# Kernel tuning notes

Hardware: AMD Instinct MI355X
Metric: run time of the kernel (lower is better)

The kernel has to match this reference:

```python
import jax, jax.numpy as jnp
import numpy as np

IN_FEATURES = 4096
OUT_FEATURES = 14336
TOKENS = 32


def setup_inputs() -> dict:
    key = jax.random.key(0)
    k1, k2, k3 = jax.random.split(key, 3)
    x = jax.random.normal(k1, (TOKENS, IN_FEATURES), dtype=jnp.float32)
    # int8-valued quantized weight stored as int32 (symmetric Q8, range [-127, 127])
    weight = jax.random.randint(k2, (OUT_FEATURES, IN_FEATURES), -127, 128, dtype=jnp.int32)
    # per-in-feature (per-column of [out,in] matrix) positive scales
    scales = jax.random.uniform(k3, (IN_FEATURES,), dtype=jnp.float32, minval=0.001, maxval=0.02)
    return {"x": x, "weight": weight, "scales": scales}


def reference(x, weight, scales):
    # Original torch: dequant[o,i] = weight[o,i] * scales[i]; out = x @ dequant.T
    # Equivalent fused form: out[t,o] = sum_i (x[t,i]*scales[i]) * weight[o,i]
    x_scaled = x * scales[None, :]            # [T, in]
    w = weight.astype(jnp.float32)            # [out, in]
    out = jnp.einsum('ti,oi->to', x_scaled, w)  # [T, out]
    return out
```

## Files before the change

kernel.cpp:

```cpp
#include <hip/hip_runtime.h>
#include <stdint.h>
#include <stddef.h>

#define IN_F   4096
#define OUT_F  14336
#define TOK    32

#define OTILE  16
#define KWAVE  (IN_F / 4)
#define KBW    (KWAVE / 32)

typedef __attribute__((ext_vector_type(8))) short bf16x8;
typedef __attribute__((ext_vector_type(4))) float f32x4;

__global__ __launch_bounds__(256) void prep_kernel(
    const float* __restrict__ x, const float* __restrict__ scales,
    int4* __restrict__ xfrag)
{
    const int f = blockIdx.x * 256 + threadIdx.x;
    const int t  = f >> 9;
    const int i8 = f & 511;
    const int kb = i8 >> 2;
    const int kg = i8 & 3;
    const float4* xp = (const float4*)(x + (size_t)t * IN_F + i8 * 8);
    const float4* sp = (const float4*)(scales + i8 * 8);
    float4 x0 = xp[0], x1 = xp[1];
    float4 s0 = sp[0], s1 = sp[1];
    float v[8] = { x0.x*s0.x, x0.y*s0.y, x0.z*s0.z, x0.w*s0.w,
                   x1.x*s1.x, x1.y*s1.y, x1.z*s1.z, x1.w*s1.w };
    uint32_t h[8];
#pragma unroll
    for (int j = 0; j < 8; ++j) {
        uint32_t b = __float_as_uint(v[j]);
        b += 0x7fffu + ((b >> 16) & 1u);
        h[j] = b >> 16;
    }
    int4 d;
    d.x = (int)(h[0] | (h[1] << 16));
    d.y = (int)(h[2] | (h[3] << 16));
    d.z = (int)(h[4] | (h[5] << 16));
    d.w = (int)(h[6] | (h[7] << 16));
    xfrag[((kb * 2 + (t >> 4)) * 64) + kg * 16 + (t & 15)] = d;
}

__global__ __launch_bounds__(256, 4) void qgemm_kernel(
    const int* __restrict__ wgt, const int4* __restrict__ xfrag,
    float* __restrict__ out)
{
    __shared__ float lred[4][8][64];
    const int lane = threadIdx.x & 63;
    const int wv   = threadIdx.x >> 6;
    const int lx   = lane & 15;
    const int quad = lane >> 4;
    const int o0   = blockIdx.x * OTILE;

    const int* wp = wgt + (size_t)(o0 + lx) * IN_F + wv * KWAVE + quad * 8;
    const int4* ap = xfrag + ((size_t)wv * KBW) * 2 * 64 + lane;

    f32x4 acc[2] = { {0.f,0.f,0.f,0.f}, {0.f,0.f,0.f,0.f} };

#pragma unroll 8
    for (int kb = 0; kb < KBW; ++kb) {
        int4 av0 = ap[(kb * 2 + 0) * 64];
        int4 av1 = ap[(kb * 2 + 1) * 64];
        const int4 w0 = *(const int4*)(wp + kb * 32);
        const int4 w1 = *(const int4*)(wp + kb * 32 + 4);
        bf16x8 b;
        b[0] = (short)(__float_as_uint((float)w0.x) >> 16);
        b[1] = (short)(__float_as_uint((float)w0.y) >> 16);
        b[2] = (short)(__float_as_uint((float)w0.z) >> 16);
        b[3] = (short)(__float_as_uint((float)w0.w) >> 16);
        b[4] = (short)(__float_as_uint((float)w1.x) >> 16);
        b[5] = (short)(__float_as_uint((float)w1.y) >> 16);
        b[6] = (short)(__float_as_uint((float)w1.z) >> 16);
        b[7] = (short)(__float_as_uint((float)w1.w) >> 16);
        bf16x8 a0, a1;
        __builtin_memcpy(&a0, &av0, 16);
        __builtin_memcpy(&a1, &av1, 16);
        acc[0] = __builtin_amdgcn_mfma_f32_16x16x32_bf16(a0, b, acc[0], 0, 0, 0);
        acc[1] = __builtin_amdgcn_mfma_f32_16x16x32_bf16(a1, b, acc[1], 0, 0, 0);
    }

#pragma unroll
    for (int s = 0; s < 8; ++s)
        lred[wv][s][lane] = acc[s >> 2][s & 3];
    __syncthreads();

    if (wv == 0) {
#pragma unroll
        for (int s = 0; s < 8; ++s) {
            const float v = lred[0][s][lane] + lred[1][s][lane]
                          + lred[2][s][lane] + lred[3][s][lane];
            const int t = (s >> 2) * 16 + quad * 4 + (s & 3);
            out[(size_t)t * OUT_F + o0 + lx] = v;
        }
    }
}

extern "C" void kernel_launch(void* const* d_in, const int* in_sizes, int n_in,
                              void* d_out, int out_size, void* d_ws, size_t ws_size,
                              hipStream_t stream)
{
    const float* x      = (const float*)d_in[0];
    const int*   wgt    = (const int*)d_in[1];
    const float* scales = (const float*)d_in[2];
    float* out = (float*)d_out;
    int4*  xfrag = (int4*)d_ws;

    prep_kernel<<<dim3((TOK * IN_F / 8) / 256), 256, 0, stream>>>(x, scales, xfrag);

    qgemm_kernel<<<dim3(OUT_F / OTILE), 256, 0, stream>>>(wgt, xfrag, out);
}
```

Before: 336.0 us.

## Stage weight tiles through double-buffered LDS via global_load_lds

Weight rows are now copied asynchronously from global memory into a double-buffered LDS tile with global_load_lds, 512 columns per chunk. Each chunk is consumed from LDS while the next one is prefetched, which replaces the per-lane strided global int4 loads. The goal is to make the weight stream (the dominant bytes, int32 weights) coalesced and overlapped with compute. In exchange the kernel adds a barrier per chunk, uses a large LDS footprint that lowers occupancy to 2 blocks per CU, and keeps the int32 weight traffic unchanged.

```diff
diff --git a/kernel.cpp b/kernel.cpp
--- a/kernel.cpp
+++ b/kernel.cpp
@@ -7,9 +7,14 @@
 #define TOK    32
 
 #define OTILE  16
-#define KWAVE  (IN_F / 4)
-#define KBW    (KWAVE / 32)
+#define CHUNK  512
+#define NCH    (IN_F / CHUNK)
+#define KBC    (CHUNK / 32)
+#define KBW    (KBC / 4)
+#define ROWPAD 516
 
+typedef const __attribute__((address_space(1))) void* gas_ptr;
+typedef __attribute__((address_space(3))) void* las_ptr;
 typedef __attribute__((ext_vector_type(8))) short bf16x8;
 typedef __attribute__((ext_vector_type(4))) float f32x4;
 
@@ -43,42 +48,67 @@
     xfrag[((kb * 2 + (t >> 4)) * 64) + kg * 16 + (t & 15)] = d;
 }
 
-__global__ __launch_bounds__(256, 4) void qgemm_kernel(
+__global__ __launch_bounds__(256, 2) void qgemm_kernel(
     const int* __restrict__ wgt, const int4* __restrict__ xfrag,
     float* __restrict__ out)
 {
+    __shared__ int   wbuf[2][OTILE * ROWPAD];
     __shared__ float lred[4][8][64];
     const int lane = threadIdx.x & 63;
     const int wv   = threadIdx.x >> 6;
+    const int wvu  = __builtin_amdgcn_readfirstlane(wv);
     const int lx   = lane & 15;
     const int quad = lane >> 4;
     const int o0   = blockIdx.x * OTILE;
 
-    const int* wp = wgt + (size_t)(o0 + lx) * IN_F + wv * KWAVE + quad * 8;
-    const int4* ap = xfrag + ((size_t)wv * KBW) * 2 * 64 + lane;
+    auto stage = [&](int buf, int c) {
+#pragma unroll
+        for (int rr = 0; rr < 4; ++rr) {
+            const int r = wvu * 4 + rr;
+            const int* src = wgt + (size_t)(o0 + r) * IN_F + c * CHUNK
+                                 + lane * 4;
+            int* dst = &wbuf[buf][r * ROWPAD];
+            __builtin_amdgcn_global_load_lds((gas_ptr)src, (las_ptr)dst, 16, 0, 0);
+            __builtin_amdgcn_global_load_lds((gas_ptr)(src + 256),
+                                             (las_ptr)(dst + 256), 16, 0, 0);
+        }
+    };
 
     f32x4 acc[2] = { {0.f,0.f,0.f,0.f}, {0.f,0.f,0.f,0.f} };
 
-#pragma unroll 8
-    for (int kb = 0; kb < KBW; ++kb) {
-        int4 av0 = ap[(kb * 2 + 0) * 64];
-        int4 av1 = ap[(kb * 2 + 1) * 64];
-        const int4 w0 = *(const int4*)(wp + kb * 32);
-        const int4 w1 = *(const int4*)(wp + kb * 32 + 4);
-        bf16x8 b;
-        b[0] = (short)(__float_as_uint((float)w0.x) >> 16);
-        b[1] = (short)(__float_as_uint((float)w0.y) >> 16);
-        b[2] = (short)(__float_as_uint((float)w0.z) >> 16);
-        b[3] = (short)(__float_as_uint((float)w0.w) >> 16);
-        b[4] = (short)(__float_as_uint((float)w1.x) >> 16);
-        b[5] = (short)(__float_as_uint((float)w1.y) >> 16);
-        b[6] = (short)(__float_as_uint((float)w1.z) >> 16);
-        b[7] = (short)(__float_as_uint((float)w1.w) >> 16);
-        bf16x8 a0, a1;
-        __builtin_memcpy(&a0, &av0, 16);
-        __builtin_memcpy(&a1, &av1, 16);
-        acc[0] = __builtin_amdgcn_mfma_f32_16x16x32_bf16(a0, b, acc[0], 0, 0, 0);
-        acc[1] = __builtin_amdgcn_mfma_f32_16x16x32_bf16(a1, b, acc[1], 0, 0, 0);
+    stage(0, 0);
+    __syncthreads();
+
+    int cur = 0;
+    for (int c = 0; c < NCH; ++c) {
+        if (c + 1 < NCH) stage(cur ^ 1, c + 1);
+
+        const int* lb = &wbuf[cur][lx * ROWPAD + quad * 8];
+#pragma unroll
+        for (int q = 0; q < KBW; ++q) {
+            const int l   = wvu * KBW + q;
+            const int kbg = c * KBC + l;
+            int4 av0 = xfrag[((size_t)kbg * 2 + 0) * 64 + lane];
+            int4 av1 = xfrag[((size_t)kbg * 2 + 1) * 64 + lane];
+            const int4 w0 = *(const int4*)(lb + l * 32);
+            const int4 w1 = *(const int4*)(lb + l * 32 + 4);
+            bf16x8 b;
+            b[0] = (short)(__float_as_uint((float)w0.x) >> 16);
+            b[1] = (short)(__float_as_uint((float)w0.y) >> 16);
+            b[2] = (short)(__float_as_uint((float)w0.z) >> 16);
+            b[3] = (short)(__float_as_uint((float)w0.w) >> 16);
+            b[4] = (short)(__float_as_uint((float)w1.x) >> 16);
+            b[5] = (short)(__float_as_uint((float)w1.y) >> 16);
+            b[6] = (short)(__float_as_uint((float)w1.z) >> 16);
+            b[7] = (short)(__float_as_uint((float)w1.w) >> 16);
+            bf16x8 a0, a1;
+            __builtin_memcpy(&a0, &av0, 16);
+            __builtin_memcpy(&a1, &av1, 16);
+            acc[0] = __builtin_amdgcn_mfma_f32_16x16x32_bf16(a0, b, acc[0], 0, 0, 0);
+            acc[1] = __builtin_amdgcn_mfma_f32_16x16x32_bf16(a1, b, acc[1], 0, 0, 0);
+        }
+        __syncthreads();
+        cur ^= 1;
     }
 
 #pragma unroll
```

After: 321.3 us. -4.4%, faster.
